# Performance work log

Measured on AMD Instinct MI355X. Metric: run time of the kernel, lower is better.

## Reference

```python
import jax, jax.numpy as jnp
import numpy as np

B, S, D, H = 8, 2048, 1024, 16
A = D // H  # attn_dim = 64
SCALE = float(np.sqrt(D))  # module divides by sqrt(d_model), NOT sqrt(attn_dim)


def setup_inputs() -> dict:
    key = jax.random.key(0)
    ks = jax.random.split(key, 6)
    # xavier-uniform bound for Linear(dim -> attn_dim)
    bound = float(np.sqrt(6.0 / (D + A)))
    return {
        "query": jax.random.normal(ks[0], (B, S, D), dtype=jnp.float32),
        "key": jax.random.normal(ks[1], (B, S, D), dtype=jnp.float32),
        "value": jax.random.normal(ks[2], (B, S, D), dtype=jnp.float32),
        "Wq": jax.random.uniform(ks[3], (D, A), jnp.float32, -bound, bound),
        "bq": jnp.zeros((A,), jnp.float32),
        "Wk": jax.random.uniform(ks[4], (D, A), jnp.float32, -bound, bound),
        "bk": jnp.zeros((A,), jnp.float32),
        "Wv": jax.random.uniform(ks[5], (D, A), jnp.float32, -bound, bound),
        "bv": jnp.zeros((A,), jnp.float32),
    }


def reference(query, key, value, Wq, bq, Wk, bk, Wv, bv):
    # Linear projections dim -> attn_dim
    q = query @ Wq + bq  # [B, S, A]
    k = key @ Wk + bk    # [B, S, A]
    v = value @ Wv + bv  # [B, S, A]
    # scaled dot-product attention; score matrix [B, S, S] is materialized
    score = jnp.einsum("bqa,bka->bqk", q, k) / SCALE
    attn = jax.nn.softmax(score, axis=-1)
    # dropout is identity in eval mode
    context = jnp.einsum("bqk,bka->bqa", attn, v)  # [B, S, A]
    return (context, attn)
```

## Files before the change

kernel.cpp:

```cpp
#include <hip/hip_runtime.h>
#include <hip/hip_bf16.h>

#define NB 8
#define SEQ 2048
#define DM 1024
#define AD 64
#define NROWS (NB * SEQ)

#define SCL2 0.04508422f

typedef __attribute__((ext_vector_type(8))) short short8;
typedef __attribute__((ext_vector_type(4))) float f32x4;

static __device__ __forceinline__ unsigned short f2bf(float f) {
    unsigned int u = __float_as_uint(f);
    u += 0x7FFFu + ((u >> 16) & 1u);
    return (unsigned short)(u >> 16);
}

static __device__ __forceinline__ f32x4 mfma16(short8 a, short8 b, f32x4 c) {
    return __builtin_amdgcn_mfma_f32_16x16x32_bf16(a, b, c, 0, 0, 0);
}

static __device__ __forceinline__ short8 pack8v(f32x4 a, f32x4 b) {
    short8 r;
    r[0] = (short)f2bf(a[0]); r[1] = (short)f2bf(a[1]);
    r[2] = (short)f2bf(a[2]); r[3] = (short)f2bf(a[3]);
    r[4] = (short)f2bf(b[0]); r[5] = (short)f2bf(b[1]);
    r[6] = (short)f2bf(b[2]); r[7] = (short)f2bf(b[3]);
    return r;
}

static __device__ __forceinline__ uint2 cvt2bf4(float4 v) {
    uint2 pk;
    pk.x = (unsigned)f2bf(v.x) | ((unsigned)f2bf(v.y) << 16);
    pk.y = (unsigned)f2bf(v.z) | ((unsigned)f2bf(v.w) << 16);
    return pk;
}

__global__ __launch_bounds__(256) void wT_kernel(
    const float* __restrict__ Wq, const float* __restrict__ Wk,
    const float* __restrict__ Wv, unsigned short* __restrict__ wT) {
    int p = blockIdx.y;
    int k0 = blockIdx.x * 64;
    const float* W = (p == 0) ? Wq : (p == 1) ? Wk : Wv;
    __shared__ unsigned short tl[64][72];
    int t = threadIdx.x;
    int c = t & 63;
    int r0 = t >> 6;
    for (int i = 0; i < 16; i++) {
        int k = r0 + i * 4;
        tl[c][k] = f2bf(W[(size_t)(k0 + k) * AD + c]);
    }
    __syncthreads();
    for (int i = 0; i < 16; i++) {
        int a = r0 + i * 4;
        wT[((size_t)p * AD + a) * DM + k0 + c] = tl[a][c];
    }
}

__global__ __launch_bounds__(256, 4) void proj_kernel(
    const float* __restrict__ q_in, const float* __restrict__ k_in,
    const float* __restrict__ v_in, const float* __restrict__ bq,
    const float* __restrict__ bk, const float* __restrict__ bv,
    const unsigned short* __restrict__ wT,
    unsigned short* __restrict__ q_out, unsigned short* __restrict__ k_out,
    unsigned short* __restrict__ vT_out) {
    int p = blockIdx.y;
    int rbase = blockIdx.x * 64;
    const float* X = (p == 0) ? q_in : (p == 1) ? k_in : v_in;
    const float* bias = (p == 0) ? bq : (p == 1) ? bk : bv;
    const unsigned short* wTp = wT + (size_t)p * AD * DM;

    __shared__ unsigned short xsb[2][64][72];
    __shared__ unsigned short wsm[2][64][72];

    int t = threadIdx.x;
    int lane = t & 63;
    int w = t >> 6;
    int arow = lane & 15;
    int agrp = lane >> 4;

    int srow = t >> 4;
    int scol = (t & 15) * 4;
    int wrow = t >> 2;
    int wcol = (t & 3) * 16;

    const float* Xb = X + (size_t)rbase * DM;

    f32x4 acc[4];
#pragma unroll
    for (int ct = 0; ct < 4; ct++) acc[ct] = (f32x4){0.f, 0.f, 0.f, 0.f};

    float4 px0, px1, px2, px3;
    float4 pw0, pw1;

    px0 = *reinterpret_cast<const float4*>(&Xb[(size_t)(0 * 16 + srow) * DM + scol]);
    px1 = *reinterpret_cast<const float4*>(&Xb[(size_t)(1 * 16 + srow) * DM + scol]);
    px2 = *reinterpret_cast<const float4*>(&Xb[(size_t)(2 * 16 + srow) * DM + scol]);
    px3 = *reinterpret_cast<const float4*>(&Xb[(size_t)(3 * 16 + srow) * DM + scol]);
    {
        const char* wp = reinterpret_cast<const char*>(wTp + (size_t)wrow * DM + wcol);
        pw0 = *reinterpret_cast<const float4*>(wp);
        pw1 = *reinterpret_cast<const float4*>(wp + 16);
    }
    *reinterpret_cast<uint2*>(&xsb[0][0 * 16 + srow][scol]) = cvt2bf4(px0);
    *reinterpret_cast<uint2*>(&xsb[0][1 * 16 + srow][scol]) = cvt2bf4(px1);
    *reinterpret_cast<uint2*>(&xsb[0][2 * 16 + srow][scol]) = cvt2bf4(px2);
    *reinterpret_cast<uint2*>(&xsb[0][3 * 16 + srow][scol]) = cvt2bf4(px3);
    *reinterpret_cast<float4*>(&wsm[0][wrow][wcol]) = pw0;
    *reinterpret_cast<float4*>(&wsm[0][wrow][wcol + 8]) = pw1;
    __syncthreads();

    for (int c = 0; c < 16; ++c) {
        int bu = c & 1;
        if (c < 15) {
            int kb = (c + 1) * 64;
            px0 = *reinterpret_cast<const float4*>(&Xb[(size_t)(0 * 16 + srow) * DM + kb + scol]);
            px1 = *reinterpret_cast<const float4*>(&Xb[(size_t)(1 * 16 + srow) * DM + kb + scol]);
            px2 = *reinterpret_cast<const float4*>(&Xb[(size_t)(2 * 16 + srow) * DM + kb + scol]);
            px3 = *reinterpret_cast<const float4*>(&Xb[(size_t)(3 * 16 + srow) * DM + kb + scol]);
            const char* wp = reinterpret_cast<const char*>(wTp + (size_t)wrow * DM + kb + wcol);
            pw0 = *reinterpret_cast<const float4*>(wp);
            pw1 = *reinterpret_cast<const float4*>(wp + 16);
        }
        const unsigned short* xr = &xsb[bu][w * 16 + arow][0];
#pragma unroll
        for (int s = 0; s < 2; ++s) {
            short8 af = *reinterpret_cast<const short8*>(&xr[s * 32 + agrp * 8]);
#pragma unroll
            for (int ct = 0; ct < 4; ++ct) {
                short8 bf = *reinterpret_cast<const short8*>(
                    &wsm[bu][ct * 16 + arow][s * 32 + agrp * 8]);
                acc[ct] = mfma16(af, bf, acc[ct]);
            }
        }
        if (c < 15) {
            int bo = bu ^ 1;
            *reinterpret_cast<uint2*>(&xsb[bo][0 * 16 + srow][scol]) = cvt2bf4(px0);
            *reinterpret_cast<uint2*>(&xsb[bo][1 * 16 + srow][scol]) = cvt2bf4(px1);
            *reinterpret_cast<uint2*>(&xsb[bo][2 * 16 + srow][scol]) = cvt2bf4(px2);
            *reinterpret_cast<uint2*>(&xsb[bo][3 * 16 + srow][scol]) = cvt2bf4(px3);
            *reinterpret_cast<float4*>(&wsm[bo][wrow][wcol]) = pw0;
            *reinterpret_cast<float4*>(&wsm[bo][wrow][wcol + 8]) = pw1;
        }
        __syncthreads();
    }

    if (p < 2) {
        unsigned short* outp = (p == 0) ? q_out : k_out;
#pragma unroll
        for (int ct = 0; ct < 4; ct++) {
            int a = ct * 16 + arow;
            float bv_ = bias[a];
#pragma unroll
            for (int rr = 0; rr < 4; rr++) {
                int row = rbase + w * 16 + agrp * 4 + rr;
                outp[(size_t)row * AD + a] = f2bf(acc[ct][rr] + bv_);
            }
        }
    } else {
        unsigned short* sc = (unsigned short*)&xsb[0][0][0];
#pragma unroll
        for (int ct = 0; ct < 4; ct++) {
            int a = ct * 16 + arow;
            float bv_ = bias[a];
#pragma unroll
            for (int rr = 0; rr < 4; rr++) {
                int row = w * 16 + agrp * 4 + rr;
                sc[a * 72 + row] = f2bf(acc[ct][rr] + bv_);
            }
        }
        __syncthreads();
        int bidx = rbase >> 11;
        int sbase = rbase & 2047;
        int rr = t & 63;
        for (int i = 0; i < 16; i++) {
            int a = (t >> 6) + i * 4;
            vT_out[((size_t)bidx * AD + a) * SEQ + sbase + rr] = sc[a * 72 + rr];
        }
    }
}

__global__ __launch_bounds__(512, 2) void attn2_kernel(
    const unsigned short* __restrict__ qb, const unsigned short* __restrict__ kb,
    const unsigned short* __restrict__ vT, float* __restrict__ attn_out,
    float* __restrict__ ctx_out) {
    int blk = blockIdx.x;
    int b = blk & 7;
    int qbase = (blk >> 3) * 32;

    __shared__ float sf[8][32][68];
    __shared__ float wsum[8][32];
    __shared__ float lr_lds[32];

    int t = threadIdx.x;
    int lane = t & 63;
    int w = t >> 6;
    int arow = lane & 15;
    int agrp = lane >> 4;

    const unsigned short* qrow = qb + ((size_t)b * SEQ + qbase) * AD;
    short8 qf0a = *reinterpret_cast<const short8*>(qrow + (size_t)arow * AD + agrp * 8);
    short8 qf1a = *reinterpret_cast<const short8*>(qrow + (size_t)arow * AD + 32 + agrp * 8);
    short8 qf0b = *reinterpret_cast<const short8*>(qrow + (size_t)(16 + arow) * AD + agrp * 8);
    short8 qf1b = *reinterpret_cast<const short8*>(qrow + (size_t)(16 + arow) * AD + 32 + agrp * 8);
    const unsigned short* kbp = kb + (size_t)b * SEQ * AD;
    const unsigned short* vTb = vT + (size_t)b * AD * SEQ;
    float* attn_b = attn_out + ((size_t)b * SEQ + qbase) * SEQ;

    int keybase = w * 256;

    float sA[4] = {0.f, 0.f, 0.f, 0.f};
    float sB[4] = {0.f, 0.f, 0.f, 0.f};
    for (int kt = 0; kt < 16; ++kt) {
        int key0 = keybase + kt * 16;
        const unsigned short* krow = kbp + (size_t)(key0 + arow) * AD;
        short8 kf0 = *reinterpret_cast<const short8*>(krow + agrp * 8);
        short8 kf1 = *reinterpret_cast<const short8*>(krow + 32 + agrp * 8);
        f32x4 aA = (f32x4){0.f, 0.f, 0.f, 0.f};
        aA = mfma16(qf0a, kf0, aA);
        aA = mfma16(qf1a, kf1, aA);
        f32x4 aB = (f32x4){0.f, 0.f, 0.f, 0.f};
        aB = mfma16(qf0b, kf0, aB);
        aB = mfma16(qf1b, kf1, aB);
#pragma unroll
        for (int r = 0; r < 4; r++) {
            sA[r] += __builtin_amdgcn_exp2f(aA[r] * SCL2);
            sB[r] += __builtin_amdgcn_exp2f(aB[r] * SCL2);
        }
    }
#pragma unroll
    for (int r = 0; r < 4; r++) {
#pragma unroll
        for (int off = 1; off < 16; off <<= 1) {
            sA[r] += __shfl_xor(sA[r], off);
            sB[r] += __shfl_xor(sB[r], off);
        }
    }
    if (arow == 0) {
#pragma unroll
        for (int r = 0; r < 4; r++) {
            wsum[w][agrp * 4 + r] = sA[r];
            wsum[w][16 + agrp * 4 + r] = sB[r];
        }
    }
    __syncthreads();
    if (t < 32) {
        float S = ((wsum[0][t] + wsum[1][t]) + (wsum[2][t] + wsum[3][t])) +
                  ((wsum[4][t] + wsum[5][t]) + (wsum[6][t] + wsum[7][t]));
        lr_lds[t] = -__builtin_amdgcn_logf(S);
    }
    __syncthreads();

    float lrA[4], lrB[4];
#pragma unroll
    for (int r = 0; r < 4; r++) {
        lrA[r] = lr_lds[agrp * 4 + r];
        lrB[r] = lr_lds[16 + agrp * 4 + r];
    }

    f32x4 caccA[4], caccB[4];
#pragma unroll
    for (int ct = 0; ct < 4; ct++) {
        caccA[ct] = (f32x4){0.f, 0.f, 0.f, 0.f};
        caccB[ct] = (f32x4){0.f, 0.f, 0.f, 0.f};
    }

    for (int g = 0; g < 4; ++g) {
        int key0b = keybase + g * 64;
#pragma unroll
        for (int kb4 = 0; kb4 < 4; ++kb4) {
            int k0 = key0b + kb4 * 16;
            const unsigned short* krow = kbp + (size_t)(k0 + arow) * AD;
            short8 kf0 = *reinterpret_cast<const short8*>(krow + agrp * 8);
            short8 kf1 = *reinterpret_cast<const short8*>(krow + 32 + agrp * 8);
            f32x4 aA = (f32x4){0.f, 0.f, 0.f, 0.f};
            aA = mfma16(qf0a, kf0, aA);
            aA = mfma16(qf1a, kf1, aA);
            f32x4 aB = (f32x4){0.f, 0.f, 0.f, 0.f};
            aB = mfma16(qf0b, kf0, aB);
            aB = mfma16(qf1b, kf1, aB);
#pragma unroll
            for (int r = 0; r < 4; r++) {
                sf[w][agrp * 4 + r][kb4 * 16 + arow] =
                    __builtin_amdgcn_exp2f(aA[r] * SCL2 + lrA[r]);
                sf[w][16 + agrp * 4 + r][kb4 * 16 + arow] =
                    __builtin_amdgcn_exp2f(aB[r] * SCL2 + lrB[r]);
            }
        }
#pragma unroll
        for (int j = 0; j < 8; ++j) {
            int row = j * 4 + agrp;
            int c4 = arow * 4;
            f32x4 vv = *reinterpret_cast<const f32x4*>(&sf[w][row][c4]);
            __builtin_nontemporal_store(
                vv, reinterpret_cast<f32x4*>(&attn_b[(size_t)row * SEQ + key0b + c4]));
        }
#pragma unroll
        for (int ks = 0; ks < 2; ++ks) {
            f32x4 pa0 = *reinterpret_cast<const f32x4*>(&sf[w][arow][ks * 32 + agrp * 8]);
            f32x4 pa1 = *reinterpret_cast<const f32x4*>(&sf[w][arow][ks * 32 + agrp * 8 + 4]);
            short8 pfA = pack8v(pa0, pa1);
            f32x4 pb0 = *reinterpret_cast<const f32x4*>(&sf[w][16 + arow][ks * 32 + agrp * 8]);
            f32x4 pb1 = *reinterpret_cast<const f32x4*>(&sf[w][16 + arow][ks * 32 + agrp * 8 + 4]);
            short8 pfB = pack8v(pb0, pb1);
#pragma unroll
            for (int ct = 0; ct < 4; ct++) {
                const unsigned short* vr =
                    vTb + (size_t)(ct * 16 + arow) * SEQ + key0b + ks * 32 + agrp * 8;
                short8 vv = *reinterpret_cast<const short8*>(vr);
                caccA[ct] = mfma16(pfA, vv, caccA[ct]);
                caccB[ct] = mfma16(pfB, vv, caccB[ct]);
            }
        }
    }

    __syncthreads();
#pragma unroll
    for (int ct = 0; ct < 4; ct++)
#pragma unroll
        for (int r = 0; r < 4; r++) {
            sf[w][agrp * 4 + r][ct * 16 + arow] = caccA[ct][r];
            sf[w][16 + agrp * 4 + r][ct * 16 + arow] = caccB[ct][r];
        }
    __syncthreads();

    float* ctx_b = ctx_out + ((size_t)b * SEQ + qbase) * AD;
    for (int i = t; i < 32 * 64; i += 512) {
        int r = i >> 6, a = i & 63;
        float v = ((sf[0][r][a] + sf[1][r][a]) + (sf[2][r][a] + sf[3][r][a])) +
                  ((sf[4][r][a] + sf[5][r][a]) + (sf[6][r][a] + sf[7][r][a]));
        __builtin_nontemporal_store(v, &ctx_b[(size_t)r * AD + a]);
    }
}

extern "C" void kernel_launch(void* const* d_in, const int* in_sizes, int n_in,
                              void* d_out, int out_size, void* d_ws, size_t ws_size,
                              hipStream_t stream) {
    const float* q_in = (const float*)d_in[0];
    const float* k_in = (const float*)d_in[1];
    const float* v_in = (const float*)d_in[2];
    const float* Wq = (const float*)d_in[3];
    const float* bq = (const float*)d_in[4];
    const float* Wk = (const float*)d_in[5];
    const float* bk = (const float*)d_in[6];
    const float* Wv = (const float*)d_in[7];
    const float* bv = (const float*)d_in[8];

    char* ws = (char*)d_ws;
    unsigned short* q_bf = (unsigned short*)(ws);
    unsigned short* k_bf = (unsigned short*)(ws + (2u << 20));
    unsigned short* vT   = (unsigned short*)(ws + (4u << 20));
    unsigned short* wT   = (unsigned short*)(ws + (6u << 20));

    float* ctx_out = (float*)d_out;
    float* attn_out = ctx_out + (size_t)NB * SEQ * AD;

    hipLaunchKernelGGL(wT_kernel, dim3(16, 3), dim3(256), 0, stream, Wq, Wk, Wv, wT);
    hipLaunchKernelGGL(proj_kernel, dim3(256, 3), dim3(256), 0, stream,
                       q_in, k_in, v_in, bq, bk, bv, wT, q_bf, k_bf, vT);
    hipLaunchKernelGGL(attn2_kernel, dim3(512), dim3(512), 0, stream,
                       q_bf, k_bf, vT, attn_out, ctx_out);
}
```

Baseline: 101.6 us.

## Split projection GEMM into 32x32 output tiles with 128-thread blocks

The projection kernel now launches 1024x3 blocks of 128 threads, each computing a 32-row by 32-column output tile instead of a 64x64 tile with 256 threads. The intent is more blocks and better CU occupancy for this phase. The V transpose store is also rewritten to use vectorized 16-byte writes. The cost is that each fp32 input row tile is now read twice, once per column half, which increases global traffic on the dominant fp32 input read.

Result: slower. 132.3 us (+30.2%).

```diff
diff --git a/kernel.cpp b/kernel.cpp
--- a/kernel.cpp
+++ b/kernel.cpp
@@ -59,7 +59,7 @@
     }
 }
 
-__global__ __launch_bounds__(256, 4) void proj_kernel(
+__global__ __launch_bounds__(128, 4) void proj_kernel(
     const float* __restrict__ q_in, const float* __restrict__ k_in,
     const float* __restrict__ v_in, const float* __restrict__ bq,
     const float* __restrict__ bk, const float* __restrict__ bv,
@@ -67,13 +67,14 @@
     unsigned short* __restrict__ q_out, unsigned short* __restrict__ k_out,
     unsigned short* __restrict__ vT_out) {
     int p = blockIdx.y;
-    int rbase = blockIdx.x * 64;
+    int rbase = (blockIdx.x >> 1) * 32;
+    int cbase = (blockIdx.x & 1) * 32;
     const float* X = (p == 0) ? q_in : (p == 1) ? k_in : v_in;
     const float* bias = (p == 0) ? bq : (p == 1) ? bk : bv;
     const unsigned short* wTp = wT + (size_t)p * AD * DM;
 
-    __shared__ unsigned short xsb[2][64][72];
-    __shared__ unsigned short wsm[2][64][72];
+    __shared__ unsigned short xsb[2][32][72];
+    __shared__ unsigned short wsm[2][32][72];
 
     int t = threadIdx.x;
     int lane = t & 63;
@@ -81,77 +82,71 @@
     int arow = lane & 15;
     int agrp = lane >> 4;
 
-    int srow = t >> 4;
-    int scol = (t & 15) * 4;
-    int wrow = t >> 2;
-    int wcol = (t & 3) * 16;
+    int sxrow = t >> 4;
+    int sxcol = (t & 15) * 4;
+    int swrow = t >> 2;
+    int swcol = (t & 3) * 16;
 
     const float* Xb = X + (size_t)rbase * DM;
-
-    f32x4 acc[4];
-#pragma unroll
-    for (int ct = 0; ct < 4; ct++) acc[ct] = (f32x4){0.f, 0.f, 0.f, 0.f};
+    const unsigned short* Wb = wTp + (size_t)cbase * DM;
+
+    f32x4 acc[2];
+    acc[0] = (f32x4){0.f, 0.f, 0.f, 0.f};
+    acc[1] = (f32x4){0.f, 0.f, 0.f, 0.f};
 
     float4 px0, px1, px2, px3;
     float4 pw0, pw1;
 
-    px0 = *reinterpret_cast<const float4*>(&Xb[(size_t)(0 * 16 + srow) * DM + scol]);
-    px1 = *reinterpret_cast<const float4*>(&Xb[(size_t)(1 * 16 + srow) * DM + scol]);
-    px2 = *reinterpret_cast<const float4*>(&Xb[(size_t)(2 * 16 + srow) * DM + scol]);
-    px3 = *reinterpret_cast<const float4*>(&Xb[(size_t)(3 * 16 + srow) * DM + scol]);
-    {
-        const char* wp = reinterpret_cast<const char*>(wTp + (size_t)wrow * DM + wcol);
-        pw0 = *reinterpret_cast<const float4*>(wp);
-        pw1 = *reinterpret_cast<const float4*>(wp + 16);
-    }
-    *reinterpret_cast<uint2*>(&xsb[0][0 * 16 + srow][scol]) = cvt2bf4(px0);
-    *reinterpret_cast<uint2*>(&xsb[0][1 * 16 + srow][scol]) = cvt2bf4(px1);
-    *reinterpret_cast<uint2*>(&xsb[0][2 * 16 + srow][scol]) = cvt2bf4(px2);
-    *reinterpret_cast<uint2*>(&xsb[0][3 * 16 + srow][scol]) = cvt2bf4(px3);
-    *reinterpret_cast<float4*>(&wsm[0][wrow][wcol]) = pw0;
-    *reinterpret_cast<float4*>(&wsm[0][wrow][wcol + 8]) = pw1;
+#define LOADSET(kb)                                                              \
+    {                                                                            \
+        px0 = *reinterpret_cast<const float4*>(&Xb[(size_t)(sxrow + 0) * DM + (kb) + sxcol]);  \
+        px1 = *reinterpret_cast<const float4*>(&Xb[(size_t)(sxrow + 8) * DM + (kb) + sxcol]);  \
+        px2 = *reinterpret_cast<const float4*>(&Xb[(size_t)(sxrow + 16) * DM + (kb) + sxcol]); \
+        px3 = *reinterpret_cast<const float4*>(&Xb[(size_t)(sxrow + 24) * DM + (kb) + sxcol]); \
+        const char* wp_ = reinterpret_cast<const char*>(&Wb[(size_t)swrow * DM + (kb) + swcol]); \
+        pw0 = *reinterpret_cast<const float4*>(wp_);                             \
+        pw1 = *reinterpret_cast<const float4*>(wp_ + 16);                        \
+    }
+
+#define WRITESET(bo)                                                             \
+    {                                                                            \
+        *reinterpret_cast<uint2*>(&xsb[bo][sxrow + 0][sxcol]) = cvt2bf4(px0);    \
+        *reinterpret_cast<uint2*>(&xsb[bo][sxrow + 8][sxcol]) = cvt2bf4(px1);    \
+        *reinterpret_cast<uint2*>(&xsb[bo][sxrow + 16][sxcol]) = cvt2bf4(px2);   \
+        *reinterpret_cast<uint2*>(&xsb[bo][sxrow + 24][sxcol]) = cvt2bf4(px3);   \
+        *reinterpret_cast<float4*>(&wsm[bo][swrow][swcol]) = pw0;                \
+        *reinterpret_cast<float4*>(&wsm[bo][swrow][swcol + 8]) = pw1;            \
+    }
+
+    LOADSET(0);
+    WRITESET(0);
     __syncthreads();
 
     for (int c = 0; c < 16; ++c) {
         int bu = c & 1;
-        if (c < 15) {
-            int kb = (c + 1) * 64;
-            px0 = *reinterpret_cast<const float4*>(&Xb[(size_t)(0 * 16 + srow) * DM + kb + scol]);
-            px1 = *reinterpret_cast<const float4*>(&Xb[(size_t)(1 * 16 + srow) * DM + kb + scol]);
-            px2 = *reinterpret_cast<const float4*>(&Xb[(size_t)(2 * 16 + srow) * DM + kb + scol]);
-            px3 = *reinterpret_cast<const float4*>(&Xb[(size_t)(3 * 16 + srow) * DM + kb + scol]);
-            const char* wp = reinterpret_cast<const char*>(wTp + (size_t)wrow * DM + kb + wcol);
-            pw0 = *reinterpret_cast<const float4*>(wp);
-            pw1 = *reinterpret_cast<const float4*>(wp + 16);
-        }
+        if (c < 15) LOADSET((c + 1) * 64);
         const unsigned short* xr = &xsb[bu][w * 16 + arow][0];
 #pragma unroll
         for (int s = 0; s < 2; ++s) {
             short8 af = *reinterpret_cast<const short8*>(&xr[s * 32 + agrp * 8]);
 #pragma unroll
-            for (int ct = 0; ct < 4; ++ct) {
+            for (int ct = 0; ct < 2; ++ct) {
                 short8 bf = *reinterpret_cast<const short8*>(
                     &wsm[bu][ct * 16 + arow][s * 32 + agrp * 8]);
                 acc[ct] = mfma16(af, bf, acc[ct]);
             }
         }
-        if (c < 15) {
-            int bo = bu ^ 1;
-            *reinterpret_cast<uint2*>(&xsb[bo][0 * 16 + srow][scol]) = cvt2bf4(px0);
-            *reinterpret_cast<uint2*>(&xsb[bo][1 * 16 + srow][scol]) = cvt2bf4(px1);
-            *reinterpret_cast<uint2*>(&xsb[bo][2 * 16 + srow][scol]) = cvt2bf4(px2);
-            *reinterpret_cast<uint2*>(&xsb[bo][3 * 16 + srow][scol]) = cvt2bf4(px3);
-            *reinterpret_cast<float4*>(&wsm[bo][wrow][wcol]) = pw0;
-            *reinterpret_cast<float4*>(&wsm[bo][wrow][wcol + 8]) = pw1;
-        }
+        if (c < 15) WRITESET(bu ^ 1);
         __syncthreads();
     }
+#undef LOADSET
+#undef WRITESET
 
     if (p < 2) {
         unsigned short* outp = (p == 0) ? q_out : k_out;
 #pragma unroll
-        for (int ct = 0; ct < 4; ct++) {
-            int a = ct * 16 + arow;
+        for (int ct = 0; ct < 2; ct++) {
+            int a = cbase + ct * 16 + arow;
             float bv_ = bias[a];
 #pragma unroll
             for (int rr = 0; rr < 4; rr++) {
@@ -162,23 +157,26 @@
     } else {
         unsigned short* sc = (unsigned short*)&xsb[0][0][0];
 #pragma unroll
-        for (int ct = 0; ct < 4; ct++) {
+        for (int ct = 0; ct < 2; ct++) {
             int a = ct * 16 + arow;
-            float bv_ = bias[a];
+            float bv_ = bias[cbase + a];
 #pragma unroll
             for (int rr = 0; rr < 4; rr++) {
                 int row = w * 16 + agrp * 4 + rr;
-                sc[a * 72 + row] = f2bf(acc[ct][rr] + bv_);
+                sc[a * 40 + row] = f2bf(acc[ct][rr] + bv_);
             }
         }
         __syncthreads();
         int bidx = rbase >> 11;
         int sbase = rbase & 2047;
-        int rr = t & 63;
-        for (int i = 0; i < 16; i++) {
-            int a = (t >> 6) + i * 4;
-            vT_out[((size_t)bidx * AD + a) * SEQ + sbase + rr] = sc[a * 72 + rr];
-        }
+        int a = t >> 2;
+        int sg = (t & 3) * 8;
+        uint2 v0 = *reinterpret_cast<const uint2*>(&sc[a * 40 + sg]);
+        uint2 v1 = *reinterpret_cast<const uint2*>(&sc[a * 40 + sg + 4]);
+        unsigned short* vrow =
+            vT_out + ((size_t)bidx * AD + cbase + a) * SEQ + sbase + sg;
+        *reinterpret_cast<uint2*>(vrow) = v0;
+        *reinterpret_cast<uint2*>(vrow + 4) = v1;
     }
 }
 
@@ -358,7 +356,7 @@
     float* attn_out = ctx_out + (size_t)NB * SEQ * AD;
 
     hipLaunchKernelGGL(wT_kernel, dim3(16, 3), dim3(256), 0, stream, Wq, Wk, Wv, wT);
-    hipLaunchKernelGGL(proj_kernel, dim3(256, 3), dim3(256), 0, stream,
+    hipLaunchKernelGGL(proj_kernel, dim3(1024, 3), dim3(128), 0, stream,
                        q_in, k_in, v_in, bq, bk, bv, wT, q_bf, k_bf, vT);
     hipLaunchKernelGGL(attn2_kernel, dim3(512), dim3(512), 0, stream,
                        q_bf, k_bf, vT, attn_out, ctx_out);
```
